# Performance work log

Measured on AMD Instinct MI355X. Metric: run time of the kernel, lower is better.

## Reference

```python
import jax, jax.numpy as jnp
import numpy as np

# dims
M, C, D = 64, 2000, 512          # clients, classes, embed_dim
H = 4                             # num_heads
HD = D // H                       # head_dim = 128
DFF = 2048                        # torch TransformerEncoderLayer default dim_feedforward
NUM_CLASSES = 2000
EPS = 1e-5


def _ln(x, g, b):
    mu = jnp.mean(x, axis=-1, keepdims=True)
    var = jnp.mean(jnp.square(x - mu), axis=-1, keepdims=True)
    return (x - mu) * jax.lax.rsqrt(var + EPS) * g + b


def setup_inputs() -> dict:
    key = jax.random.key(0)
    ks = jax.random.split(key, 16)
    s = 0.02
    return {
        "client_protos": jax.random.normal(ks[0], (M, C, D), jnp.float32),
        "norm_g": jnp.ones((D,), jnp.float32),
        "norm_b": jnp.zeros((D,), jnp.float32),
        "in_proj_w": jax.random.normal(ks[1], (3 * D, D), jnp.float32) * s,
        "in_proj_b": jnp.zeros((3 * D,), jnp.float32),
        "out_proj_w": jax.random.normal(ks[2], (D, D), jnp.float32) * s,
        "out_proj_b": jnp.zeros((D,), jnp.float32),
        "lin1_w": jax.random.normal(ks[3], (DFF, D), jnp.float32) * s,
        "lin1_b": jnp.zeros((DFF,), jnp.float32),
        "lin2_w": jax.random.normal(ks[4], (D, DFF), jnp.float32) * s,
        "lin2_b": jnp.zeros((D,), jnp.float32),
        "norm1_g": jnp.ones((D,), jnp.float32),
        "norm1_b": jnp.zeros((D,), jnp.float32),
        "norm2_g": jnp.ones((D,), jnp.float32),
        "norm2_b": jnp.zeros((D,), jnp.float32),
        "global_query": jax.random.normal(ks[5], (NUM_CLASSES, D), jnp.float32),
        "all_labels": jax.random.randint(ks[6], (C,), 0, NUM_CLASSES, jnp.int32),
        "round_num": 10,
        "client_idx": 0,
    }


def reference(client_protos, norm_g, norm_b, in_proj_w, in_proj_b,
              out_proj_w, out_proj_b, lin1_w, lin1_b, lin2_w, lin2_b,
              norm1_g, norm1_b, norm2_g, norm2_b, global_query,
              all_labels, round_num, client_idx):
    # 1) LayerNorm over all prototypes: (M, C, D)
    x = _ln(client_protos, norm_g, norm_b)
    # 2) Per-class transformer: original loops c in range(C) on (1, M, D).
    #    Batched: treat C as batch -> (C, M, D). Post-norm torch encoder layer.
    x = jnp.transpose(x, (1, 0, 2))  # (C, M, D)
    # self-attention
    qkv = x @ in_proj_w.T + in_proj_b          # (C, M, 3D)
    q, k, v = jnp.split(qkv, 3, axis=-1)
    q = q.reshape(C, M, H, HD)
    k = k.reshape(C, M, H, HD)
    v = v.reshape(C, M, H, HD)
    scores = jnp.einsum('cqhd,ckhd->chqk', q, k) / np.sqrt(HD).astype(np.float32)
    attn = jax.nn.softmax(scores, axis=-1)
    sa = jnp.einsum('chqk,ckhd->cqhd', attn, v).reshape(C, M, D)
    sa = sa @ out_proj_w.T + out_proj_b
    x = _ln(x + sa, norm1_g, norm1_b)
    # feed-forward (relu, dropout = eval no-op)
    ff = jax.nn.relu(x @ lin1_w.T + lin1_b) @ lin2_w.T + lin2_b
    x = _ln(x + ff, norm2_g, norm2_b)           # (C, M, D) == protos_trans^T
    # 3) Cross-attention with per-class global query
    q_all = global_query[all_labels].reshape(C, H, HD)
    kv_all = x.reshape(C, M, H, HD)
    s2 = jnp.einsum('chd,cmhd->chm', q_all, kv_all) / np.sqrt(HD).astype(np.float32)
    w2 = jax.nn.softmax(s2, axis=-1)
    attn_out = jnp.einsum('chm,cmhd->chd', w2, kv_all).reshape(C, D)
    return attn_out
```

## Files before the change

### kernel.cpp

```cpp
#include <hip/hip_runtime.h>

typedef _Float16 f16;
typedef _Float16 half4 __attribute__((ext_vector_type(4)));
typedef _Float16 half8 __attribute__((ext_vector_type(8)));
typedef float f32x4 __attribute__((ext_vector_type(4)));

typedef __attribute__((address_space(1))) void* as1v;
typedef __attribute__((address_space(3))) void* as3v;

#define SCALE 0.08838834764831845f

static __device__ __forceinline__ f32x4 mfma16(half8 a, half8 b, f32x4 c){
  return __builtin_amdgcn_mfma_f32_16x16x32_f16(a, b, c, 0, 0, 0);
}

__global__ __launch_bounds__(256) void k_cvt(const float* __restrict__ src, f16* __restrict__ dst, int n){
  int i = (blockIdx.x * 256 + threadIdx.x) * 8;
  if (i >= n) return;
  float4 a = *(const float4*)(src + i);
  float4 b = *(const float4*)(src + i + 4);
  half8 h;
  h[0] = (f16)a.x; h[1] = (f16)a.y; h[2] = (f16)a.z; h[3] = (f16)a.w;
  h[4] = (f16)b.x; h[5] = (f16)b.y; h[6] = (f16)b.z; h[7] = (f16)b.w;
  *(half8*)(dst + i) = h;
}

__global__ __launch_bounds__(256) void k_ln0(const float* __restrict__ protos,
                                             const float* __restrict__ g,
                                             const float* __restrict__ bb,
                                             f16* __restrict__ xb, int c0){
  const int w = threadIdx.x >> 6, l = threadIdx.x & 63;
  const int q = blockIdx.x * 4 + w;
  const int cl = q >> 6, m = q & 63;
  const float* in = protos + ((size_t)m * 2000 + (size_t)(c0 + cl)) * 512;
  const int d0 = l * 8;
  float4 a = *(const float4*)(in + d0);
  float4 c = *(const float4*)(in + d0 + 4);
  float s  = a.x + a.y + a.z + a.w + c.x + c.y + c.z + c.w;
  float ss = a.x*a.x + a.y*a.y + a.z*a.z + a.w*a.w + c.x*c.x + c.y*c.y + c.z*c.z + c.w*c.w;
#pragma unroll
  for (int msk = 1; msk < 64; msk <<= 1){ s += __shfl_xor(s, msk); ss += __shfl_xor(ss, msk); }
  const float mu = s * (1.f/512.f);
  const float rs = rsqrtf(ss * (1.f/512.f) - mu*mu + 1e-5f);
  float4 g0 = *(const float4*)(g + d0),  g1 = *(const float4*)(g + d0 + 4);
  float4 b0 = *(const float4*)(bb + d0), b1 = *(const float4*)(bb + d0 + 4);
  half8 o;
  o[0] = (f16)((a.x - mu) * rs * g0.x + b0.x);
  o[1] = (f16)((a.y - mu) * rs * g0.y + b0.y);
  o[2] = (f16)((a.z - mu) * rs * g0.z + b0.z);
  o[3] = (f16)((a.w - mu) * rs * g0.w + b0.w);
  o[4] = (f16)((c.x - mu) * rs * g1.x + b1.x);
  o[5] = (f16)((c.y - mu) * rs * g1.y + b1.y);
  o[6] = (f16)((c.z - mu) * rs * g1.z + b1.z);
  o[7] = (f16)((c.w - mu) * rs * g1.w + b1.w);
  *(half8*)(xb + (size_t)q * 512 + d0) = o;
}

__global__ __launch_bounds__(256) void k_resln(const f16* __restrict__ t, const f16* __restrict__ skip,
                                               const float* __restrict__ g, const float* __restrict__ bb,
                                               f16* __restrict__ outp){
  const int w = threadIdx.x >> 6, l = threadIdx.x & 63;
  const size_t q = (size_t)blockIdx.x * 4 + w;
  const int d0 = l * 8;
  half8 tv = *(const half8*)(t + q * 512 + d0);
  half8 sk = *(const half8*)(skip + q * 512 + d0);
  float v0 = (float)tv[0] + (float)sk[0], v1 = (float)tv[1] + (float)sk[1];
  float v2 = (float)tv[2] + (float)sk[2], v3 = (float)tv[3] + (float)sk[3];
  float v4 = (float)tv[4] + (float)sk[4], v5 = (float)tv[5] + (float)sk[5];
  float v6 = (float)tv[6] + (float)sk[6], v7 = (float)tv[7] + (float)sk[7];
  float s  = v0+v1+v2+v3+v4+v5+v6+v7;
  float ss = v0*v0+v1*v1+v2*v2+v3*v3+v4*v4+v5*v5+v6*v6+v7*v7;
#pragma unroll
  for (int msk = 1; msk < 64; msk <<= 1){ s += __shfl_xor(s, msk); ss += __shfl_xor(ss, msk); }
  const float mu = s * (1.f/512.f);
  const float rs = rsqrtf(ss * (1.f/512.f) - mu*mu + 1e-5f);
  float4 g0 = *(const float4*)(g + d0),  g1 = *(const float4*)(g + d0 + 4);
  float4 b0 = *(const float4*)(bb + d0), b1 = *(const float4*)(bb + d0 + 4);
  half8 o;
  o[0] = (f16)((v0 - mu) * rs * g0.x + b0.x);
  o[1] = (f16)((v1 - mu) * rs * g0.y + b0.y);
  o[2] = (f16)((v2 - mu) * rs * g0.z + b0.z);
  o[3] = (f16)((v3 - mu) * rs * g0.w + b0.w);
  o[4] = (f16)((v4 - mu) * rs * g1.x + b1.x);
  o[5] = (f16)((v5 - mu) * rs * g1.y + b1.y);
  o[6] = (f16)((v6 - mu) * rs * g1.z + b1.z);
  o[7] = (f16)((v7 - mu) * rs * g1.w + b1.w);
  *(half8*)(outp + q * 512 + d0) = o;
}

#define GLL(gp, lp) __builtin_amdgcn_global_load_lds((as1v)(void*)(gp), (as3v)(lp), 16, 0, 0)

template<bool RELU>
__global__ __launch_bounds__(512, 2) void k_gemm(const f16* __restrict__ A, const f16* __restrict__ B,
                                                 const float* __restrict__ bias, f16* __restrict__ Cout,
                                                 int N, int K, int gn){
  extern __shared__ char smem_raw[];
  f16* lds = (f16*)smem_raw;

  const int t = threadIdx.x, w = t >> 6, l = t & 63;
  const int wr = w >> 2, wc = w & 3;

  const int nwg = gridDim.x;
  const int q8 = nwg >> 3, r8 = nwg & 7;
  const int xcd = blockIdx.x & 7, lidx = blockIdx.x >> 3;
  const int swz = (xcd < r8 ? xcd * (q8 + 1) : r8 * (q8 + 1) + (xcd - r8) * q8) + lidx;
  const int tm = swz / gn, tn = swz % gn;
  const size_t row0 = (size_t)tm * 256;
  const int col0 = tn * 256;

  f32x4 acc[8][4];
#pragma unroll
  for (int m = 0; m < 8; ++m)
#pragma unroll
    for (int n = 0; n < 4; ++n) acc[m][n] = (f32x4){0.f,0.f,0.f,0.f};

  const int lsw = ((t & 7) ^ ((t >> 3) & 7)) * 8;
  const f16* gAb = A + (row0 + (size_t)(t >> 3)) * (size_t)K + lsw;
  const f16* gBb = B + ((size_t)col0 + (size_t)(t >> 3)) * (size_t)K + lsw;
  const int t8 = t * 8;

  const int rA  = (l & 15) * 64;
  const int ps0 = (((l >> 4) ^ (l & 7)) << 3);
  const int ps1 = (((4 + (l >> 4)) ^ (l & 7)) << 3);
  const int abase = wr * 8192 + rA;
  const int bbase = 16384 + wc * 4096 + rA;

  const int NT = K >> 6;

  auto stgA = [&](int tt, int h){
    f16* d = lds + (tt & 1) * 32768 + h * 8192 + t8;
    const f16* s = gAb + (size_t)(h * 128) * K + (size_t)tt * 64;
    GLL(s, d);
    GLL(s + (size_t)64 * K, d + 4096);
  };
  auto stgB = [&](int tt, int h){
    f16* d = lds + (tt & 1) * 32768 + 16384 + h * 8192 + t8;
    const f16* s = gBb + (size_t)(h * 128) * K + (size_t)tt * 64;
    GLL(s, d);
    GLL(s + (size_t)64 * K, d + 4096);
  };

  stgA(0, 0); stgA(0, 1); stgB(0, 0); stgB(0, 1);
  if (NT > 1){
    stgA(1, 0);
    asm volatile("s_waitcnt vmcnt(2)" ::: "memory");
  } else {
    asm volatile("s_waitcnt vmcnt(0)" ::: "memory");
  }
  __builtin_amdgcn_s_barrier();

  for (int tt = 0; tt < NT; ++tt){
    const f16* sb = lds + (tt & 1) * 32768;
    const bool s1 = tt + 1 < NT, s2 = tt + 2 < NT;
    half8 af03[4][2], af47[4][2], bf[4][2];

#pragma unroll
    for (int m = 0; m < 4; ++m){
      af03[m][0] = *(const half8*)(sb + abase + m * 1024 + ps0);
      af03[m][1] = *(const half8*)(sb + abase + m * 1024 + ps1);
    }
#pragma unroll
    for (int n = 0; n < 2; ++n){
      bf[n][0] = *(const half8*)(sb + bbase + n * 1024 + ps0);
      bf[n][1] = *(const half8*)(sb + bbase + n * 1024 + ps1);
    }
    if (s1) stgA(tt + 1, 1);
    __builtin_amdgcn_s_barrier();
    asm volatile("s_waitcnt lgkmcnt(0)" ::: "memory");
    __builtin_amdgcn_sched_barrier(0);
    __builtin_amdgcn_s_setprio(1);
#pragma unroll
    for (int ks = 0; ks < 2; ++ks)
#pragma unroll
      for (int m = 0; m < 4; ++m)
#pragma unroll
        for (int n = 0; n < 2; ++n)
          acc[m][n] = mfma16(bf[n][ks], af03[m][ks], acc[m][n]);
    __builtin_amdgcn_s_setprio(0);
    __builtin_amdgcn_s_barrier();

#pragma unroll
    for (int n = 2; n < 4; ++n){
      bf[n][0] = *(const half8*)(sb + bbase + n * 1024 + ps0);
      bf[n][1] = *(const half8*)(sb + bbase + n * 1024 + ps1);
    }
    if (s1) stgB(tt + 1, 0);
    __builtin_amdgcn_s_barrier();
    asm volatile("s_waitcnt lgkmcnt(0)" ::: "memory");
    __builtin_amdgcn_sched_barrier(0);
    __builtin_amdgcn_s_setprio(1);
#pragma unroll
    for (int ks = 0; ks < 2; ++ks)
#pragma unroll
      for (int m = 0; m < 4; ++m)
#pragma unroll
        for (int n = 2; n < 4; ++n)
          acc[m][n] = mfma16(bf[n][ks], af03[m][ks], acc[m][n]);
    __builtin_amdgcn_s_setprio(0);
    __builtin_amdgcn_s_barrier();

#pragma unroll
    for (int m = 0; m < 4; ++m){
      af47[m][0] = *(const half8*)(sb + abase + (m + 4) * 1024 + ps0);
      af47[m][1] = *(const half8*)(sb + abase + (m + 4) * 1024 + ps1);
    }
    if (s1) stgB(tt + 1, 1);
    __builtin_amdgcn_s_barrier();
    asm volatile("s_waitcnt lgkmcnt(0)" ::: "memory");
    __builtin_amdgcn_sched_barrier(0);
    __builtin_amdgcn_s_setprio(1);
#pragma unroll
    for (int ks = 0; ks < 2; ++ks)
#pragma unroll
      for (int m = 0; m < 4; ++m)
#pragma unroll
        for (int n = 0; n < 2; ++n)
          acc[m + 4][n] = mfma16(bf[n][ks], af47[m][ks], acc[m + 4][n]);
    __builtin_amdgcn_s_setprio(0);
    __builtin_amdgcn_s_barrier();

    if (s2) stgA(tt + 2, 0);
    __builtin_amdgcn_s_barrier();
    __builtin_amdgcn_s_setprio(1);
#pragma unroll
    for (int ks = 0; ks < 2; ++ks)
#pragma unroll
      for (int m = 0; m < 4; ++m)
#pragma unroll
        for (int n = 2; n < 4; ++n)
          acc[m + 4][n] = mfma16(bf[n][ks], af47[m][ks], acc[m + 4][n]);
    __builtin_amdgcn_s_setprio(0);
    if (s1){
      if (s2) { asm volatile("s_waitcnt vmcnt(2)" ::: "memory"); }
      else    { asm volatile("s_waitcnt vmcnt(0)" ::: "memory"); }
    }
    __builtin_amdgcn_s_barrier();
  }

#pragma unroll
  for (int n = 0; n < 4; ++n){
    const int c = col0 + wc * 64 + n * 16 + ((l >> 4) << 2);
    float4 b4 = *(const float4*)(bias + c);
#pragma unroll
    for (int m = 0; m < 8; ++m){
      const size_t r = row0 + (size_t)(wr * 128 + m * 16 + (l & 15));
      float v0 = acc[m][n][0] + b4.x;
      float v1 = acc[m][n][1] + b4.y;
      float v2 = acc[m][n][2] + b4.z;
      float v3 = acc[m][n][3] + b4.w;
      if (RELU){ v0 = fmaxf(v0, 0.f); v1 = fmaxf(v1, 0.f); v2 = fmaxf(v2, 0.f); v3 = fmaxf(v3, 0.f); }
      half4 h; h[0] = (f16)v0; h[1] = (f16)v1; h[2] = (f16)v2; h[3] = (f16)v3;
      *(half4*)&Cout[r * (size_t)N + c] = h;
    }
  }
}

__global__ __launch_bounds__(256) void k_attn(const f16* __restrict__ qkv, f16* __restrict__ sa){
  __shared__ __align__(16) f16 P[4][4096];
  __shared__ __align__(16) f16 VT[4][4096];
  const int cl = blockIdx.x;
  const int h = threadIdx.x >> 6, l = threadIdx.x & 63;
  const f16* base = qkv + (size_t)cl * 64 * 1536;
  const f16* Qp = base + h * 128;
  const f16* Kp = base + 512 + h * 128;
  const f16* Vp = base + 1024 + h * 128;

  f32x4 s[4][4];
#pragma unroll
  for (int x = 0; x < 4; ++x)
#pragma unroll
    for (int y = 0; y < 4; ++y) s[x][y] = (f32x4){0.f,0.f,0.f,0.f};
#pragma unroll
  for (int ks = 0; ks < 4; ++ks){
    half8 aq[4], bk[4];
#pragma unroll
    for (int x = 0; x < 4; ++x)
      aq[x] = *(const half8*)&Qp[(size_t)(x * 16 + (l & 15)) * 1536 + ks * 32 + (l >> 4) * 8];
#pragma unroll
    for (int y = 0; y < 4; ++y)
      bk[y] = *(const half8*)&Kp[(size_t)(y * 16 + (l & 15)) * 1536 + ks * 32 + (l >> 4) * 8];
#pragma unroll
    for (int x = 0; x < 4; ++x)
#pragma unroll
      for (int y = 0; y < 4; ++y)
        s[x][y] = mfma16(aq[x], bk[y], s[x][y]);
  }

  char* Pb = (char*)&P[h][0];
#pragma unroll
  for (int x = 0; x < 4; ++x){
#pragma unroll
    for (int j = 0; j < 4; ++j){
      float e0 = s[x][0][j] * SCALE;
      float e1 = s[x][1][j] * SCALE;
      float e2 = s[x][2][j] * SCALE;
      float e3 = s[x][3][j] * SCALE;
      float mx = fmaxf(fmaxf(e0, e1), fmaxf(e2, e3));
#pragma unroll
      for (int msk = 1; msk < 16; msk <<= 1) mx = fmaxf(mx, __shfl_xor(mx, msk));
      e0 = __expf(e0 - mx); e1 = __expf(e1 - mx); e2 = __expf(e2 - mx); e3 = __expf(e3 - mx);
      float sm = e0 + e1 + e2 + e3;
#pragma unroll
      for (int msk = 1; msk < 16; msk <<= 1) sm += __shfl_xor(sm, msk);
      const float inv = 1.f / sm;
      const int row = x * 16 + (l >> 4) * 4 + j;
      const int rb = row * 128 + (l & 15) * 2;
      const int rsw = (row & 7) << 4;
      *(f16*)(Pb + ((rb     ) ^ rsw)) = (f16)(e0 * inv);
      *(f16*)(Pb + ((rb + 32) ^ rsw)) = (f16)(e1 * inv);
      *(f16*)(Pb + ((rb + 64) ^ rsw)) = (f16)(e2 * inv);
      *(f16*)(Pb + ((rb + 96) ^ rsw)) = (f16)(e3 * inv);
    }
  }

  char* Vb = (char*)&VT[h][0];
#pragma unroll
  for (int dh = 0; dh < 2; ++dh){
#pragma unroll
    for (int it = 0; it < 8; ++it){
      const int chunk = it * 64 + l;
      const int m = chunk >> 3, dc = chunk & 7;
      half8 v = *(const half8*)&Vp[(size_t)m * 1536 + dh * 64 + dc * 8];
#pragma unroll
      for (int jj = 0; jj < 8; ++jj){
        const int dd = dc * 8 + jj;
        *(f16*)(Vb + ((dd * 128 + m * 2) ^ ((dd & 7) << 4))) = v[jj];
      }
    }
    __syncthreads();
#pragma unroll
    for (int x = 0; x < 4; ++x){
      const int ar = x * 16 + (l & 15);
      const int ab = ar * 128, sw = (ar & 7) << 4;
      half8 ap0 = *(const half8*)(Pb + ((ab + (l >> 4) * 16) ^ sw));
      half8 ap1 = *(const half8*)(Pb + ((ab + 64 + (l >> 4) * 16) ^ sw));
#pragma unroll
      for (int dt = 0; dt < 4; ++dt){
        const int vr = dt * 16 + (l & 15);
        const int vb = vr * 128, vsw = (vr & 7) << 4;
        half8 b0 = *(const half8*)(Vb + ((vb + (l >> 4) * 16) ^ vsw));
        half8 b1 = *(const half8*)(Vb + ((vb + 64 + (l >> 4) * 16) ^ vsw));
        f32x4 o = (f32x4){0.f,0.f,0.f,0.f};
        o = mfma16(ap0, b0, o);
        o = mfma16(ap1, b1, o);
#pragma unroll
        for (int j = 0; j < 4; ++j){
          const int mrow = x * 16 + (l >> 4) * 4 + j;
          const int dcol = dh * 64 + dt * 16 + (l & 15);
          sa[((size_t)cl * 64 + mrow) * 512 + h * 128 + dcol] = (f16)o[j];
        }
      }
    }
    __syncthreads();
  }
}

#define ZOFF(m, cb) (((m) * 1024 + (cb)) ^ (((m) & 31) << 4))
__global__ __launch_bounds__(256) void k_resln_cross(const f16* __restrict__ t, const f16* __restrict__ skip,
                                                     const float* __restrict__ g, const float* __restrict__ bb,
                                                     const float* __restrict__ gq, const int* __restrict__ labels,
                                                     float* __restrict__ out, int c0){
  __shared__ __align__(16) char Z[65536];
  const int cl = blockIdx.x;
  const int w = threadIdx.x >> 6, l = threadIdx.x & 63;
  const int cg = c0 + cl;
  const size_t rbase = (size_t)cl * 64 * 512;
  const int d0 = l * 8;

  float4 g0 = *(const float4*)(g + d0),  g1 = *(const float4*)(g + d0 + 4);
  float4 b0 = *(const float4*)(bb + d0), b1 = *(const float4*)(bb + d0 + 4);

#pragma unroll 4
  for (int i = 0; i < 16; ++i){
    const int m = w * 16 + i;
    const size_t q = rbase + (size_t)m * 512;
    half8 tv = *(const half8*)(t + q + d0);
    half8 sk = *(const half8*)(skip + q + d0);
    float v0 = (float)tv[0] + (float)sk[0], v1 = (float)tv[1] + (float)sk[1];
    float v2 = (float)tv[2] + (float)sk[2], v3 = (float)tv[3] + (float)sk[3];
    float v4 = (float)tv[4] + (float)sk[4], v5 = (float)tv[5] + (float)sk[5];
    float v6 = (float)tv[6] + (float)sk[6], v7 = (float)tv[7] + (float)sk[7];
    float s  = v0+v1+v2+v3+v4+v5+v6+v7;
    float ss = v0*v0+v1*v1+v2*v2+v3*v3+v4*v4+v5*v5+v6*v6+v7*v7;
#pragma unroll
    for (int msk = 1; msk < 64; msk <<= 1){ s += __shfl_xor(s, msk); ss += __shfl_xor(ss, msk); }
    const float mu = s * (1.f/512.f);
    const float rs = rsqrtf(ss * (1.f/512.f) - mu*mu + 1e-5f);
    half8 o;
    o[0] = (f16)((v0 - mu) * rs * g0.x + b0.x);
    o[1] = (f16)((v1 - mu) * rs * g0.y + b0.y);
    o[2] = (f16)((v2 - mu) * rs * g0.z + b0.z);
    o[3] = (f16)((v3 - mu) * rs * g0.w + b0.w);
    o[4] = (f16)((v4 - mu) * rs * g1.x + b1.x);
    o[5] = (f16)((v5 - mu) * rs * g1.y + b1.y);
    o[6] = (f16)((v6 - mu) * rs * g1.z + b1.z);
    o[7] = (f16)((v7 - mu) * rs * g1.w + b1.w);
    *(half8*)(Z + ZOFF(m, l * 16)) = o;
  }
  __syncthreads();

  const int h = w;
  const float* q = gq + (size_t)labels[cg] * 512 + h * 128;
  float s = 0.f;
#pragma unroll
  for (int d = 0; d < 128; d += 8){
    half8 v = *(const half8*)(Z + ZOFF(l, (h * 128 + d) * 2));
    float4 q0 = *(const float4*)&q[d];
    float4 q1 = *(const float4*)&q[d + 4];
    s += q0.x*(float)v[0] + q0.y*(float)v[1] + q0.z*(float)v[2] + q0.w*(float)v[3]
       + q1.x*(float)v[4] + q1.y*(float)v[5] + q1.z*(float)v[6] + q1.w*(float)v[7];
  }
  s *= SCALE;
  float mx = s;
#pragma unroll
  for (int msk = 1; msk < 64; msk <<= 1) mx = fmaxf(mx, __shfl_xor(mx, msk));
  float e = __expf(s - mx);
  float sm = e;
#pragma unroll
  for (int msk = 1; msk < 64; msk <<= 1) sm += __shfl_xor(sm, msk);
  const float wgt = e / sm;

  float a0 = 0.f, a1 = 0.f;
  for (int m = 0; m < 64; ++m){
    const float wm = __shfl(wgt, m);
    const f16* zm = (const f16*)(Z + ZOFF(m, (h * 128 + 2 * l) * 2));
    a0 += wm * (float)zm[0];
    a1 += wm * (float)zm[1];
  }
  float2 o; o.x = a0; o.y = a1;
  *(float2*)&out[(size_t)cg * 512 + h * 128 + 2 * l] = o;
}

extern "C" void kernel_launch(void* const* d_in, const int* in_sizes, int n_in,
                              void* d_out, int out_size, void* d_ws, size_t ws_size,
                              hipStream_t stream){
  (void)in_sizes; (void)n_in; (void)out_size;
  const float* protos = (const float*)d_in[0];
  const float* norm_g = (const float*)d_in[1];
  const float* norm_b = (const float*)d_in[2];
  const float* in_w   = (const float*)d_in[3];
  const float* in_b   = (const float*)d_in[4];
  const float* ow     = (const float*)d_in[5];
  const float* ob     = (const float*)d_in[6];
  const float* l1w    = (const float*)d_in[7];
  const float* l1b    = (const float*)d_in[8];
  const float* l2w    = (const float*)d_in[9];
  const float* l2b    = (const float*)d_in[10];
  const float* n1g    = (const float*)d_in[11];
  const float* n1b    = (const float*)d_in[12];
  const float* n2g    = (const float*)d_in[13];
  const float* n2b    = (const float*)d_in[14];
  const float* gq     = (const float*)d_in[15];
  const int*   labels = (const int*)d_in[16];
  float* out = (float*)d_out;

  char* p = (char*)d_ws;
  auto alloc = [&](size_t bytes)->char*{
    char* r = p; p += (bytes + 255) & ~(size_t)255; return r;
  };
  f16* Wq = (f16*)alloc((size_t)1536*512*2);
  f16* Wo = (f16*)alloc((size_t)512*512*2);
  f16* W1 = (f16*)alloc((size_t)2048*512*2);
  f16* W2 = (f16*)alloc((size_t)512*2048*2);
  const size_t fixed = (size_t)(p - (char*)d_ws);

  const size_t per_class = (size_t)64*512*2 + (size_t)64*2048*2 + (size_t)64*512*2 + (size_t)64*512*2;
  long long avail = (long long)ws_size - (long long)fixed - 8192;
  long long cc_max = avail > 0 ? avail / (long long)per_class : 0;
  int Cc = (int)(cc_max > 2000 ? 2000 : cc_max);
  Cc &= ~3;
  if (Cc < 4) Cc = 4;

  f16* xb  = (f16*)alloc((size_t)Cc*64*512*2);
  f16* big = (f16*)alloc((size_t)Cc*64*2048*2);
  f16* sac = (f16*)alloc((size_t)Cc*64*512*2);
  f16* tmp = (f16*)alloc((size_t)Cc*64*512*2);

  k_cvt<<<1536*512/2048, 256, 0, stream>>>(in_w, Wq, 1536*512);
  k_cvt<<<512*512/2048,  256, 0, stream>>>(ow,   Wo, 512*512);
  k_cvt<<<2048*512/2048, 256, 0, stream>>>(l1w,  W1, 2048*512);
  k_cvt<<<2048*512/2048, 256, 0, stream>>>(l2w,  W2, 512*2048);

  const size_t SMEM = 131072;
  for (int c0 = 0; c0 < 2000; c0 += Cc){
    const int cc = (2000 - c0 < Cc) ? (2000 - c0) : Cc;
    const int R = cc * 64;
    const int gm = R / 256;
    k_ln0<<<R/4, 256, 0, stream>>>(protos, norm_g, norm_b, xb, c0);
    k_gemm<false><<<gm*6, 512, SMEM, stream>>>(xb, Wq, in_b, big, 1536, 512, 6);
    k_attn<<<cc, 256, 0, stream>>>(big, sac);
    k_gemm<false><<<gm*2, 512, SMEM, stream>>>(sac, Wo, ob, tmp, 512, 512, 2);
    k_resln<<<R/4, 256, 0, stream>>>(tmp, xb, n1g, n1b, sac);
    k_gemm<true><<<gm*8, 512, SMEM, stream>>>(sac, W1, l1b, big, 2048, 512, 8);
    k_gemm<false><<<gm*2, 512, SMEM, stream>>>(big, W2, l2b, tmp, 512, 2048, 2);
    k_resln_cross<<<cc, 256, 0, stream>>>(tmp, sac, n2g, n2b, gq, labels, out, c0);
  }
}
```

Measured before the change: 1.437 ms.

## Switch GEMM to 32x32x16 MFMA with k-slab LDS layout

Replaces the 16x16x32 MFMA tiles in the main GEMM with 32x32x16 MFMA instructions, so each wave issues fewer, larger matrix ops per k-step. The global-to-LDS staging is reorganised: each thread now loads a row-contiguous 8-element chunk into k-slab-major LDS, dropping the XOR swizzle. The aim is to raise matrix-core throughput and cut LDS fragment reads. It risks LDS bank conflicts from the unswizzled layout, and the epilogue is rewritten for the 32x32 accumulator layout.

Result: slower. 1.856 ms (+29.1%).

```diff
diff --git a/kernel.cpp b/kernel.cpp
--- a/kernel.cpp
+++ b/kernel.cpp
@@ -4,6 +4,7 @@
 typedef _Float16 half4 __attribute__((ext_vector_type(4)));
 typedef _Float16 half8 __attribute__((ext_vector_type(8)));
 typedef float f32x4 __attribute__((ext_vector_type(4)));
+typedef float f32x16 __attribute__((ext_vector_type(16)));
 
 typedef __attribute__((address_space(1))) void* as1v;
 typedef __attribute__((address_space(3))) void* as3v;
@@ -12,6 +13,9 @@
 
 static __device__ __forceinline__ f32x4 mfma16(half8 a, half8 b, f32x4 c){
   return __builtin_amdgcn_mfma_f32_16x16x32_f16(a, b, c, 0, 0, 0);
+}
+static __device__ __forceinline__ f32x16 mfma32(half8 a, half8 b, f32x16 c){
+  return __builtin_amdgcn_mfma_f32_32x32x16_f16(a, b, c, 0, 0, 0);
 }
 
 __global__ __launch_bounds__(256) void k_cvt(const float* __restrict__ src, f16* __restrict__ dst, int n){
@@ -108,36 +112,36 @@
   const size_t row0 = (size_t)tm * 256;
   const int col0 = tn * 256;
 
-  f32x4 acc[8][4];
-#pragma unroll
-  for (int m = 0; m < 8; ++m)
-#pragma unroll
-    for (int n = 0; n < 4; ++n) acc[m][n] = (f32x4){0.f,0.f,0.f,0.f};
-
-  const int lsw = ((t & 7) ^ ((t >> 3) & 7)) * 8;
-  const f16* gAb = A + (row0 + (size_t)(t >> 3)) * (size_t)K + lsw;
-  const f16* gBb = B + ((size_t)col0 + (size_t)(t >> 3)) * (size_t)K + lsw;
+  f32x16 acc[4][2];
+#pragma unroll
+  for (int m = 0; m < 4; ++m)
+#pragma unroll
+    for (int n = 0; n < 2; ++n)
+#pragma unroll
+      for (int j = 0; j < 16; ++j) acc[m][n][j] = 0.f;
+
+  const f16* gAt = A + (row0 + (size_t)(t & 255)) * (size_t)K + ((t >> 8) << 3);
+  const f16* gBt = B + ((size_t)col0 + (size_t)(t & 255)) * (size_t)K + ((t >> 8) << 3);
   const int t8 = t * 8;
 
-  const int rA  = (l & 15) * 64;
-  const int ps0 = (((l >> 4) ^ (l & 7)) << 3);
-  const int ps1 = (((4 + (l >> 4)) ^ (l & 7)) << 3);
-  const int abase = wr * 8192 + rA;
-  const int bbase = 16384 + wc * 4096 + rA;
+  const int lso = (l >> 5) * 2048;
+  const int lro = (l & 31) * 8;
+  const int abase = lso + wr * 1024 + lro;
+  const int bbase = 16384 + lso + wc * 512 + lro;
 
   const int NT = K >> 6;
 
   auto stgA = [&](int tt, int h){
     f16* d = lds + (tt & 1) * 32768 + h * 8192 + t8;
-    const f16* s = gAb + (size_t)(h * 128) * K + (size_t)tt * 64;
+    const f16* s = gAt + (size_t)tt * 64 + h * 32;
     GLL(s, d);
-    GLL(s + (size_t)64 * K, d + 4096);
+    GLL(s + 16, d + 4096);
   };
   auto stgB = [&](int tt, int h){
     f16* d = lds + (tt & 1) * 32768 + 16384 + h * 8192 + t8;
-    const f16* s = gBb + (size_t)(h * 128) * K + (size_t)tt * 64;
+    const f16* s = gBt + (size_t)tt * 64 + h * 32;
     GLL(s, d);
-    GLL(s + (size_t)64 * K, d + 4096);
+    GLL(s + 16, d + 4096);
   };
 
   stgA(0, 0); stgA(0, 1); stgB(0, 0); stgB(0, 1);
@@ -152,70 +156,60 @@
   for (int tt = 0; tt < NT; ++tt){
     const f16* sb = lds + (tt & 1) * 32768;
     const bool s1 = tt + 1 < NT, s2 = tt + 2 < NT;
-    half8 af03[4][2], af47[4][2], bf[4][2];
-
-#pragma unroll
-    for (int m = 0; m < 4; ++m){
-      af03[m][0] = *(const half8*)(sb + abase + m * 1024 + ps0);
-      af03[m][1] = *(const half8*)(sb + abase + m * 1024 + ps1);
-    }
-#pragma unroll
-    for (int n = 0; n < 2; ++n){
-      bf[n][0] = *(const half8*)(sb + bbase + n * 1024 + ps0);
-      bf[n][1] = *(const half8*)(sb + bbase + n * 1024 + ps1);
-    }
+    half8 af01[2][4], af23[2][4], bf[2][4];
+
+#pragma unroll
+    for (int m = 0; m < 2; ++m)
+#pragma unroll
+      for (int ks = 0; ks < 4; ++ks)
+        af01[m][ks] = *(const half8*)(sb + abase + m * 256 + ks * 4096);
+#pragma unroll
+    for (int ks = 0; ks < 4; ++ks)
+      bf[0][ks] = *(const half8*)(sb + bbase + ks * 4096);
     if (s1) stgA(tt + 1, 1);
     __builtin_amdgcn_s_barrier();
     asm volatile("s_waitcnt lgkmcnt(0)" ::: "memory");
     __builtin_amdgcn_sched_barrier(0);
     __builtin_amdgcn_s_setprio(1);
 #pragma unroll
-    for (int ks = 0; ks < 2; ++ks)
-#pragma unroll
-      for (int m = 0; m < 4; ++m)
-#pragma unroll
-        for (int n = 0; n < 2; ++n)
-          acc[m][n] = mfma16(bf[n][ks], af03[m][ks], acc[m][n]);
+    for (int ks = 0; ks < 4; ++ks)
+#pragma unroll
+      for (int m = 0; m < 2; ++m)
+        acc[m][0] = mfma32(bf[0][ks], af01[m][ks], acc[m][0]);
     __builtin_amdgcn_s_setprio(0);
     __builtin_amdgcn_s_barrier();
 
 #pragma unroll
-    for (int n = 2; n < 4; ++n){
-      bf[n][0] = *(const half8*)(sb + bbase + n * 1024 + ps0);
-      bf[n][1] = *(const half8*)(sb + bbase + n * 1024 + ps1);
-    }
+    for (int ks = 0; ks < 4; ++ks)
+      bf[1][ks] = *(const half8*)(sb + bbase + 256 + ks * 4096);
     if (s1) stgB(tt + 1, 0);
     __builtin_amdgcn_s_barrier();
     asm volatile("s_waitcnt lgkmcnt(0)" ::: "memory");
     __builtin_amdgcn_sched_barrier(0);
     __builtin_amdgcn_s_setprio(1);
 #pragma unroll
-    for (int ks = 0; ks < 2; ++ks)
-#pragma unroll
-      for (int m = 0; m < 4; ++m)
-#pragma unroll
-        for (int n = 2; n < 4; ++n)
-          acc[m][n] = mfma16(bf[n][ks], af03[m][ks], acc[m][n]);
+    for (int ks = 0; ks < 4; ++ks)
+#pragma unroll
+      for (int m = 0; m < 2; ++m)
+        acc[m][1] = mfma32(bf[1][ks], af01[m][ks], acc[m][1]);
     __builtin_amdgcn_s_setprio(0);
     __builtin_amdgcn_s_barrier();
 
 #pragma unroll
-    for (int m = 0; m < 4; ++m){
-      af47[m][0] = *(const half8*)(sb + abase + (m + 4) * 1024 + ps0);
-      af47[m][1] = *(const half8*)(sb + abase + (m + 4) * 1024 + ps1);
-    }
+    for (int m = 0; m < 2; ++m)
+#pragma unroll
+      for (int ks = 0; ks < 4; ++ks)
+        af23[m][ks] = *(const half8*)(sb + abase + (m + 2) * 256 + ks * 4096);
     if (s1) stgB(tt + 1, 1);
     __builtin_amdgcn_s_barrier();
     asm volatile("s_waitcnt lgkmcnt(0)" ::: "memory");
     __builtin_amdgcn_sched_barrier(0);
     __builtin_amdgcn_s_setprio(1);
 #pragma unroll
-    for (int ks = 0; ks < 2; ++ks)
-#pragma unroll
-      for (int m = 0; m < 4; ++m)
-#pragma unroll
-        for (int n = 0; n < 2; ++n)
-          acc[m + 4][n] = mfma16(bf[n][ks], af47[m][ks], acc[m + 4][n]);
+    for (int ks = 0; ks < 4; ++ks)
+#pragma unroll
+      for (int m = 0; m < 2; ++m)
+        acc[m + 2][0] = mfma32(bf[0][ks], af23[m][ks], acc[m + 2][0]);
     __builtin_amdgcn_s_setprio(0);
     __builtin_amdgcn_s_barrier();
 
@@ -223,12 +217,10 @@
     __builtin_amdgcn_s_barrier();
     __builtin_amdgcn_s_setprio(1);
 #pragma unroll
-    for (int ks = 0; ks < 2; ++ks)
-#pragma unroll
-      for (int m = 0; m < 4; ++m)
-#pragma unroll
-        for (int n = 2; n < 4; ++n)
-          acc[m + 4][n] = mfma16(bf[n][ks], af47[m][ks], acc[m + 4][n]);
+    for (int ks = 0; ks < 4; ++ks)
+#pragma unroll
+      for (int m = 0; m < 2; ++m)
+        acc[m + 2][1] = mfma32(bf[1][ks], af23[m][ks], acc[m + 2][1]);
     __builtin_amdgcn_s_setprio(0);
     if (s1){
       if (s2) { asm volatile("s_waitcnt vmcnt(2)" ::: "memory"); }
@@ -238,19 +230,22 @@
   }
 
 #pragma unroll
-  for (int n = 0; n < 4; ++n){
-    const int c = col0 + wc * 64 + n * 16 + ((l >> 4) << 2);
-    float4 b4 = *(const float4*)(bias + c);
-#pragma unroll
-    for (int m = 0; m < 8; ++m){
-      const size_t r = row0 + (size_t)(wr * 128 + m * 16 + (l & 15));
-      float v0 = acc[m][n][0] + b4.x;
-      float v1 = acc[m][n][1] + b4.y;
-      float v2 = acc[m][n][2] + b4.z;
-      float v3 = acc[m][n][3] + b4.w;
-      if (RELU){ v0 = fmaxf(v0, 0.f); v1 = fmaxf(v1, 0.f); v2 = fmaxf(v2, 0.f); v3 = fmaxf(v3, 0.f); }
-      half4 h; h[0] = (f16)v0; h[1] = (f16)v1; h[2] = (f16)v2; h[3] = (f16)v3;
-      *(half4*)&Cout[r * (size_t)N + c] = h;
+  for (int n = 0; n < 2; ++n){
+#pragma unroll
+    for (int q = 0; q < 4; ++q){
+      const int c = col0 + wc * 64 + n * 32 + q * 8 + ((l >> 5) << 2);
+      float4 b4 = *(const float4*)(bias + c);
+#pragma unroll
+      for (int m = 0; m < 4; ++m){
+        const size_t r = row0 + (size_t)(wr * 128 + m * 32 + (l & 31));
+        float v0 = acc[m][n][q * 4 + 0] + b4.x;
+        float v1 = acc[m][n][q * 4 + 1] + b4.y;
+        float v2 = acc[m][n][q * 4 + 2] + b4.z;
+        float v3 = acc[m][n][q * 4 + 3] + b4.w;
+        if (RELU){ v0 = fmaxf(v0, 0.f); v1 = fmaxf(v1, 0.f); v2 = fmaxf(v2, 0.f); v3 = fmaxf(v3, 0.f); }
+        half4 h; h[0] = (f16)v0; h[1] = (f16)v1; h[2] = (f16)v2; h[3] = (f16)v3;
+        *(half4*)&Cout[r * (size_t)N + c] = h;
+      }
     }
   }
 }
```
